# Kernel tuning notes

Hardware: AMD Instinct MI355X
Metric: run time of the kernel (lower is better)

Reference implementation:

```python
import jax, jax.numpy as jnp
import numpy as np

B, C = 4096, 1024  # batch_size, label_size (== embedding_dim of dense outputs)


def setup_inputs() -> dict:
    key = jax.random.key(0)
    k1, k2, k3 = jax.random.split(key, 3)
    return {
        "outs": jax.random.normal(k1, (B, C), dtype=jnp.float32),
        "class_centers": jax.random.normal(k2, (C, C), dtype=jnp.float32),
        "batch_label": jax.random.randint(k3, (B,), 0, C, dtype=jnp.int32),
    }


def reference(outs, class_centers, batch_label):
    b, c = outs.shape
    # ---- standard cross-entropy (F.cross_entropy, mean reduction) ----
    logp = jax.nn.log_softmax(outs, axis=-1)
    ce = -jnp.mean(jnp.take_along_axis(logp, batch_label[:, None].astype(jnp.int32), axis=1))

    # ---- InfoNCE with Wasserstein hard-negative mining ----
    # memory bank stores detached embeddings -> centers carry no gradient
    centers = jax.lax.stop_gradient(class_centers)
    pos = centers[batch_label]  # [B, C] positive per anchor

    # calculate_2_wasserstein_dist on 1-D vectors reduces EXACTLY to
    # ||x - y||^2 - 2*d*sqrt(1e-15)  (covariance terms vanish for a single column)
    const = jnp.float32(-2.0 * c * np.sqrt(1e-15))
    x = jax.lax.stop_gradient(outs)  # similarity used only for index selection
    sq = jnp.sum(x * x, axis=-1)  # [B]
    sim = sq[:, None] + sq[None, :] - 2.0 * (x @ x.T) + const  # [B, B]

    # negatives: different label (self automatically excluded: same label)
    mask = batch_label[:, None] != batch_label[None, :]  # [B, B]
    neg_inf = jnp.float32(-1e30)
    # hard negative: largest wasserstein distance among negatives (topk k=1)
    hard_idx = jnp.argmax(jnp.where(mask, sim, neg_inf), axis=1)  # [B]
    # random negative: uniform over negatives via Gumbel-max (torch randperm analogue)
    g = jax.random.gumbel(jax.random.key(42), (b, b), dtype=jnp.float32)
    rand_idx = jnp.argmax(jnp.where(mask, g, neg_inf), axis=1)  # [B]

    pos_sim = jnp.sum(outs * pos, axis=-1)                # [B]
    n_rand = jnp.sum(outs * outs[rand_idx], axis=-1)      # [B]
    n_hard = jnp.sum(outs * outs[hard_idx], axis=-1)      # [B]
    logits = jnp.stack([pos_sim, n_rand, n_hard], axis=1)  # [B, 1+num_negatives]
    info_nce = -jnp.mean(jax.nn.log_softmax(logits, axis=1)[:, 0])

    return ce + 0.1 * info_nce
```

## Files before the change

kernel.cpp:

```cpp
#include <hip/hip_runtime.h>
#include <hip/hip_bf16.h>
#include <stdint.h>

#define Bsz 4096
#define Csz 1024

typedef __attribute__((ext_vector_type(8))) short short8;
typedef __attribute__((ext_vector_type(4))) float f32x4;

__device__ __forceinline__ unsigned fenc(float v) {
  unsigned u = __float_as_uint(v);
  return (u & 0x80000000u) ? ~u : (u | 0x80000000u);
}

__device__ __forceinline__ void load_lds16(const void* g, void* l) {
  __builtin_amdgcn_global_load_lds(
      (const __attribute__((address_space(1))) void*)g,
      (__attribute__((address_space(3))) void*)l, 16, 0, 0);
}

__device__ __forceinline__ uint32_t rotl32(uint32_t x, int r) {
  return (x << r) | (x >> (32 - r));
}

__global__ __launch_bounds__(256) void k_rowstats(
    const float* __restrict__ outs, const int* __restrict__ label,
    unsigned short* __restrict__ xb, float* __restrict__ sq,
    float* __restrict__ ce) {
  const int row = blockIdx.x;
  const int tid = threadIdx.x;
  const int lane = tid & 63, wid = tid >> 6;
  const float4 v = reinterpret_cast<const float4*>(outs + (size_t)row * Csz)[tid];

  ushort4 u4;
  {
    __hip_bfloat16 h;
    h = __float2bfloat16(v.x); u4.x = *reinterpret_cast<const unsigned short*>(&h);
    h = __float2bfloat16(v.y); u4.y = *reinterpret_cast<const unsigned short*>(&h);
    h = __float2bfloat16(v.z); u4.z = *reinterpret_cast<const unsigned short*>(&h);
    h = __float2bfloat16(v.w); u4.w = *reinterpret_cast<const unsigned short*>(&h);
  }
  reinterpret_cast<ushort4*>(xb + (size_t)row * Csz)[tid] = u4;

  __shared__ float wred[3][4];
  float mx = fmaxf(fmaxf(v.x, v.y), fmaxf(v.z, v.w));
#pragma unroll
  for (int off = 32; off; off >>= 1) mx = fmaxf(mx, __shfl_xor(mx, off, 64));
  if (lane == 0) wred[0][wid] = mx;
  __syncthreads();
  mx = fmaxf(fmaxf(wred[0][0], wred[0][1]), fmaxf(wred[0][2], wred[0][3]));

  float se = expf(v.x - mx) + expf(v.y - mx) + expf(v.z - mx) + expf(v.w - mx);
  float s2 = v.x * v.x + v.y * v.y + v.z * v.z + v.w * v.w;
#pragma unroll
  for (int off = 32; off; off >>= 1) {
    se += __shfl_xor(se, off, 64);
    s2 += __shfl_xor(s2, off, 64);
  }
  if (lane == 0) { wred[1][wid] = se; wred[2][wid] = s2; }
  __syncthreads();
  if (tid == 0) {
    const float set = wred[1][0] + wred[1][1] + wred[1][2] + wred[1][3];
    const float sqt = wred[2][0] + wred[2][1] + wred[2][2] + wred[2][3];
    sq[row] = sqt;
    ce[row] = -(outs[(size_t)row * Csz + label[row]] - mx - logf(set));
  }
}

__global__ __launch_bounds__(256) void k_hard(
    const unsigned short* __restrict__ xb, const float* __restrict__ sq,
    const int* __restrict__ label, unsigned long long* __restrict__ hard) {
  __shared__ unsigned short As[128 * 64];
  __shared__ unsigned short Bs[128 * 64];

  int rem = blockIdx.x, bi = 0;
  while (rem >= 32 - bi) { rem -= 32 - bi; ++bi; }
  const int bj = bi + rem;

  const int tid = threadIdx.x;
  const int wid = tid >> 6, lane = tid & 63;
  const int wr = wid >> 1, wc = wid & 1;
  const int fr = lane & 15;
  const int fq = lane >> 4;
  const int sx = lane & 7;

  f32x4 acc[4][4];
#pragma unroll
  for (int m = 0; m < 4; ++m)
#pragma unroll
    for (int n = 0; n < 4; ++n) acc[m][n] = (f32x4){0.f, 0.f, 0.f, 0.f};

  const unsigned short* Ag = xb + (size_t)(bi * 128) * Csz;
  const unsigned short* Bg = xb + (size_t)(bj * 128) * Csz;
  const int lrow = lane >> 3;
  const int lch = ((lane & 7) ^ lrow) * 8;

  for (int kt = 0; kt < Csz; kt += 64) {
#pragma unroll
    for (int c = 0; c < 4; ++c) {
      const int r = wid * 32 + c * 8;
      load_lds16(Ag + (size_t)(r + lrow) * Csz + kt + lch, &As[r * 64]);
      load_lds16(Bg + (size_t)(r + lrow) * Csz + kt + lch, &Bs[r * 64]);
    }
    __syncthreads();
#pragma unroll
    for (int ks = 0; ks < 2; ++ks) {
      const int choff = ((ks * 4 + fq) ^ sx) * 8;
      short8 a[4], b[4];
#pragma unroll
      for (int m = 0; m < 4; ++m)
        a[m] = *reinterpret_cast<const short8*>(
            &As[(wr * 64 + m * 16 + fr) * 64 + choff]);
#pragma unroll
      for (int n = 0; n < 4; ++n)
        b[n] = *reinterpret_cast<const short8*>(
            &Bs[(wc * 64 + n * 16 + fr) * 64 + choff]);
#pragma unroll
      for (int m = 0; m < 4; ++m)
#pragma unroll
        for (int n = 0; n < 4; ++n)
          acc[m][n] = __builtin_amdgcn_mfma_f32_16x16x32_bf16(a[m], b[n], acc[m][n], 0, 0, 0);
    }
    __syncthreads();
  }

  const float cst = -2.0f * 1024.0f * 3.1622776601683794e-8f;

#pragma unroll
  for (int m = 0; m < 4; ++m) {
#pragma unroll
    for (int r = 0; r < 4; ++r) {
      const int i = bi * 128 + wr * 64 + m * 16 + fq * 4 + r;
      const int li = label[i];
      const float sqi = sq[i];
      float bestv = -3.0e38f;
      int bestj = 0x7FFFFFFF;
#pragma unroll
      for (int n = 0; n < 4; ++n) {
        const int j = bj * 128 + wc * 64 + n * 16 + fr;
        const float val = sqi + sq[j] - 2.0f * acc[m][n][r] + cst;
        if (label[j] != li && val > bestv) { bestv = val; bestj = j; }
      }
      unsigned long long pack =
          (bestj == 0x7FFFFFFF)
              ? 0ull
              : (((unsigned long long)fenc(bestv)) << 32) | (unsigned)(~bestj);
#pragma unroll
      for (int off = 1; off < 16; off <<= 1) {
        unsigned long long o = __shfl_xor(pack, off, 64);
        if (o > pack) pack = o;
      }
      if (fr == 0 && pack) atomicMax(&hard[i], pack);
    }
  }

  if (bi != bj) {
#pragma unroll
    for (int n = 0; n < 4; ++n) {
      const int j = bj * 128 + wc * 64 + n * 16 + fr;
      const int lj = label[j];
      const float sqj = sq[j];
      unsigned long long pack = 0ull;
#pragma unroll
      for (int m = 0; m < 4; ++m) {
#pragma unroll
        for (int r = 0; r < 4; ++r) {
          const int i = bi * 128 + wr * 64 + m * 16 + fq * 4 + r;
          if (label[i] != lj) {
            const float val = sq[i] + sqj - 2.0f * acc[m][n][r] + cst;
            const unsigned long long p =
                (((unsigned long long)fenc(val)) << 32) | (unsigned)(~i);
            if (p > pack) pack = p;
          }
        }
      }
      unsigned long long o;
      o = __shfl_xor(pack, 16, 64); if (o > pack) pack = o;
      o = __shfl_xor(pack, 32, 64); if (o > pack) pack = o;
      if (fq == 0 && pack) atomicMax(&hard[j], pack);
    }
  }
}

__global__ __launch_bounds__(256) void k_rand(
    const int* __restrict__ label, int* __restrict__ ridx) {
  const int i = blockIdx.x;
  const int tid = threadIdx.x;
  const int lane = tid & 63, wid = tid >> 6;
  const int li0 = label[i], li1 = label[i + 2048];
  const uint32_t k1c = 42u, k2c = 0x1BD11BDAu ^ 42u;
  unsigned long long b0 = 0ull, b1 = 0ull;
  for (int j = tid; j < Bsz; j += 256) {
    uint32_t x0 = (uint32_t)(i * Bsz + j);
    uint32_t x1 = x0 + 8388608u;
    x1 += k1c;
#define RND(rt) { x0 += x1; x1 = rotl32(x1, rt); x1 ^= x0; }
    RND(13) RND(15) RND(26) RND(6)
    x0 += k1c; x1 += k2c + 1u;
    RND(17) RND(29) RND(16) RND(24)
    x0 += k2c; x1 += 2u;
    RND(13) RND(15) RND(26) RND(6)
    x1 += k1c + 3u;
    RND(17) RND(29) RND(16) RND(24)
    x0 += k1c; x1 += k2c + 4u;
    RND(13) RND(15) RND(26) RND(6)
    x0 += k2c; x1 += 5u;
#undef RND
    const int lj = label[j];
    if (lj != li0) {
      unsigned long long p = (((unsigned long long)(x0 >> 9)) << 32) | (uint32_t)(~j);
      if (p > b0) b0 = p;
    }
    if (lj != li1) {
      unsigned long long p = (((unsigned long long)(x1 >> 9)) << 32) | (uint32_t)(~j);
      if (p > b1) b1 = p;
    }
  }
#pragma unroll
  for (int off = 32; off; off >>= 1) {
    unsigned long long o0 = __shfl_xor(b0, off, 64); if (o0 > b0) b0 = o0;
    unsigned long long o1 = __shfl_xor(b1, off, 64); if (o1 > b1) b1 = o1;
  }
  __shared__ unsigned long long r0[4], r1[4];
  if (lane == 0) { r0[wid] = b0; r1[wid] = b1; }
  __syncthreads();
  if (tid == 0) {
#pragma unroll
    for (int w = 1; w < 4; ++w) {
      if (r0[w] > b0) b0 = r0[w];
      if (r1[w] > b1) b1 = r1[w];
    }
    ridx[i] = (int)(~(uint32_t)b0);
    ridx[i + 2048] = (int)(~(uint32_t)b1);
  }
}

__global__ __launch_bounds__(256) void k_nce(
    const float* __restrict__ outs, const float* __restrict__ centers,
    const int* __restrict__ label, const unsigned long long* __restrict__ hard,
    const int* __restrict__ ridx, float* __restrict__ nce) {
  const int i = blockIdx.x;
  const int tid = threadIdx.x;
  const int lane = tid & 63, wid = tid >> 6;
  const int li = label[i];
  const int jh = (int)(~(uint32_t)hard[i]);
  const int jr = ridx[i];
  const float4 a  = reinterpret_cast<const float4*>(outs + (size_t)i * Csz)[tid];
  const float4 c  = reinterpret_cast<const float4*>(centers + (size_t)li * Csz)[tid];
  const float4 rr = reinterpret_cast<const float4*>(outs + (size_t)jr * Csz)[tid];
  const float4 hh = reinterpret_cast<const float4*>(outs + (size_t)jh * Csz)[tid];
  float dp = a.x * c.x + a.y * c.y + a.z * c.z + a.w * c.w;
  float dr = a.x * rr.x + a.y * rr.y + a.z * rr.z + a.w * rr.w;
  float dh = a.x * hh.x + a.y * hh.y + a.z * hh.z + a.w * hh.w;
#pragma unroll
  for (int off = 32; off; off >>= 1) {
    dp += __shfl_xor(dp, off, 64);
    dr += __shfl_xor(dr, off, 64);
    dh += __shfl_xor(dh, off, 64);
  }
  __shared__ float w0[4], w1[4], w2[4];
  if (lane == 0) { w0[wid] = dp; w1[wid] = dr; w2[wid] = dh; }
  __syncthreads();
  if (tid == 0) {
    const float l0 = w0[0] + w0[1] + w0[2] + w0[3];
    const float l1 = w1[0] + w1[1] + w1[2] + w1[3];
    const float l2 = w2[0] + w2[1] + w2[2] + w2[3];
    const float m = fmaxf(l0, fmaxf(l1, l2));
    const float lse = logf(expf(l0 - m) + expf(l1 - m) + expf(l2 - m));
    nce[i] = -(l0 - m - lse);
  }
}

__global__ __launch_bounds__(1024) void k_final(
    const float* __restrict__ ce, const float* __restrict__ nce,
    float* __restrict__ out) {
  __shared__ double s[1024];
  const int tid = threadIdx.x;
  double v = 0.0;
#pragma unroll
  for (int q = 0; q < 4; ++q) {
    v += (double)ce[tid + q * 1024];
    v += 0.1 * (double)nce[tid + q * 1024];
  }
  s[tid] = v;
  __syncthreads();
  for (int off = 512; off; off >>= 1) {
    if (tid < off) s[tid] += s[tid + off];
    __syncthreads();
  }
  if (tid == 0) out[0] = (float)(s[0] / 4096.0);
}

extern "C" void kernel_launch(void* const* d_in, const int* in_sizes, int n_in,
                              void* d_out, int out_size, void* d_ws, size_t ws_size,
                              hipStream_t stream) {
  const float* outs = (const float*)d_in[0];
  const float* centers = (const float*)d_in[1];
  const int* label = (const int*)d_in[2];
  float* out = (float*)d_out;

  char* ws = (char*)d_ws;
  unsigned short* xb = (unsigned short*)ws;
  unsigned long long* hard = (unsigned long long*)(ws + (8u << 20));
  float* sq = (float*)(ws + (8u << 20) + 32768);
  float* ce = sq + Bsz;
  float* nce = ce + Bsz;
  int* ridx = (int*)(nce + Bsz);

  hipMemsetAsync(hard, 0, Bsz * sizeof(unsigned long long), stream);
  k_rowstats<<<Bsz, 256, 0, stream>>>(outs, label, xb, sq, ce);
  k_hard<<<528, 256, 0, stream>>>(xb, sq, label, hard);
  k_rand<<<Bsz / 2, 256, 0, stream>>>(label, ridx);
  k_nce<<<Bsz, 256, 0, stream>>>(outs, centers, label, hard, ridx, nce);
  k_final<<<1, 1024, 0, stream>>>(ce, nce, out);
}
```

Baseline: 171.9 us.

## Fuse memset and random-negative kernel into rowstats; per-wave direct-load Gram tiles

Folds the hard-buffer zeroing and the Gumbel random-index computation into the row-stats kernel, which removes a memset and a separate launch. The Gram kernel is rewritten so each wave owns a 64x64 upper-triangular tile. Each wave loads bf16 operands straight from global memory into registers with double buffering, with no LDS or block barriers, and a swizzled block order aims to improve L2 locality. The cost is no operand sharing through LDS, so global/L2 traffic per MFMA is higher and far more atomics go out from the smaller tiles.

```diff
diff --git a/kernel.cpp b/kernel.cpp
--- a/kernel.cpp
+++ b/kernel.cpp
@@ -13,12 +13,6 @@
   return (u & 0x80000000u) ? ~u : (u | 0x80000000u);
 }
 
-__device__ __forceinline__ void load_lds16(const void* g, void* l) {
-  __builtin_amdgcn_global_load_lds(
-      (const __attribute__((address_space(1))) void*)g,
-      (__attribute__((address_space(3))) void*)l, 16, 0, 0);
-}
-
 __device__ __forceinline__ uint32_t rotl32(uint32_t x, int r) {
   return (x << r) | (x >> (32 - r));
 }
@@ -26,7 +20,8 @@
 __global__ __launch_bounds__(256) void k_rowstats(
     const float* __restrict__ outs, const int* __restrict__ label,
     unsigned short* __restrict__ xb, float* __restrict__ sq,
-    float* __restrict__ ce) {
+    float* __restrict__ ce, unsigned long long* __restrict__ hard,
+    int* __restrict__ ridx) {
   const int row = blockIdx.x;
   const int tid = threadIdx.x;
   const int lane = tid & 63, wid = tid >> 6;
@@ -64,129 +59,12 @@
     const float sqt = wred[2][0] + wred[2][1] + wred[2][2] + wred[2][3];
     sq[row] = sqt;
     ce[row] = -(outs[(size_t)row * Csz + label[row]] - mx - logf(set));
-  }
-}
-
-__global__ __launch_bounds__(256) void k_hard(
-    const unsigned short* __restrict__ xb, const float* __restrict__ sq,
-    const int* __restrict__ label, unsigned long long* __restrict__ hard) {
-  __shared__ unsigned short As[128 * 64];
-  __shared__ unsigned short Bs[128 * 64];
-
-  int rem = blockIdx.x, bi = 0;
-  while (rem >= 32 - bi) { rem -= 32 - bi; ++bi; }
-  const int bj = bi + rem;
-
-  const int tid = threadIdx.x;
-  const int wid = tid >> 6, lane = tid & 63;
-  const int wr = wid >> 1, wc = wid & 1;
-  const int fr = lane & 15;
-  const int fq = lane >> 4;
-  const int sx = lane & 7;
-
-  f32x4 acc[4][4];
-#pragma unroll
-  for (int m = 0; m < 4; ++m)
-#pragma unroll
-    for (int n = 0; n < 4; ++n) acc[m][n] = (f32x4){0.f, 0.f, 0.f, 0.f};
-
-  const unsigned short* Ag = xb + (size_t)(bi * 128) * Csz;
-  const unsigned short* Bg = xb + (size_t)(bj * 128) * Csz;
-  const int lrow = lane >> 3;
-  const int lch = ((lane & 7) ^ lrow) * 8;
-
-  for (int kt = 0; kt < Csz; kt += 64) {
-#pragma unroll
-    for (int c = 0; c < 4; ++c) {
-      const int r = wid * 32 + c * 8;
-      load_lds16(Ag + (size_t)(r + lrow) * Csz + kt + lch, &As[r * 64]);
-      load_lds16(Bg + (size_t)(r + lrow) * Csz + kt + lch, &Bs[r * 64]);
-    }
-    __syncthreads();
-#pragma unroll
-    for (int ks = 0; ks < 2; ++ks) {
-      const int choff = ((ks * 4 + fq) ^ sx) * 8;
-      short8 a[4], b[4];
-#pragma unroll
-      for (int m = 0; m < 4; ++m)
-        a[m] = *reinterpret_cast<const short8*>(
-            &As[(wr * 64 + m * 16 + fr) * 64 + choff]);
-#pragma unroll
-      for (int n = 0; n < 4; ++n)
-        b[n] = *reinterpret_cast<const short8*>(
-            &Bs[(wc * 64 + n * 16 + fr) * 64 + choff]);
-#pragma unroll
-      for (int m = 0; m < 4; ++m)
-#pragma unroll
-        for (int n = 0; n < 4; ++n)
-          acc[m][n] = __builtin_amdgcn_mfma_f32_16x16x32_bf16(a[m], b[n], acc[m][n], 0, 0, 0);
-    }
-    __syncthreads();
-  }
-
-  const float cst = -2.0f * 1024.0f * 3.1622776601683794e-8f;
-
-#pragma unroll
-  for (int m = 0; m < 4; ++m) {
-#pragma unroll
-    for (int r = 0; r < 4; ++r) {
-      const int i = bi * 128 + wr * 64 + m * 16 + fq * 4 + r;
-      const int li = label[i];
-      const float sqi = sq[i];
-      float bestv = -3.0e38f;
-      int bestj = 0x7FFFFFFF;
-#pragma unroll
-      for (int n = 0; n < 4; ++n) {
-        const int j = bj * 128 + wc * 64 + n * 16 + fr;
-        const float val = sqi + sq[j] - 2.0f * acc[m][n][r] + cst;
-        if (label[j] != li && val > bestv) { bestv = val; bestj = j; }
-      }
-      unsigned long long pack =
-          (bestj == 0x7FFFFFFF)
-              ? 0ull
-              : (((unsigned long long)fenc(bestv)) << 32) | (unsigned)(~bestj);
-#pragma unroll
-      for (int off = 1; off < 16; off <<= 1) {
-        unsigned long long o = __shfl_xor(pack, off, 64);
-        if (o > pack) pack = o;
-      }
-      if (fr == 0 && pack) atomicMax(&hard[i], pack);
-    }
-  }
-
-  if (bi != bj) {
-#pragma unroll
-    for (int n = 0; n < 4; ++n) {
-      const int j = bj * 128 + wc * 64 + n * 16 + fr;
-      const int lj = label[j];
-      const float sqj = sq[j];
-      unsigned long long pack = 0ull;
-#pragma unroll
-      for (int m = 0; m < 4; ++m) {
-#pragma unroll
-        for (int r = 0; r < 4; ++r) {
-          const int i = bi * 128 + wr * 64 + m * 16 + fq * 4 + r;
-          if (label[i] != lj) {
-            const float val = sq[i] + sqj - 2.0f * acc[m][n][r] + cst;
-            const unsigned long long p =
-                (((unsigned long long)fenc(val)) << 32) | (unsigned)(~i);
-            if (p > pack) pack = p;
-          }
-        }
-      }
-      unsigned long long o;
-      o = __shfl_xor(pack, 16, 64); if (o > pack) pack = o;
-      o = __shfl_xor(pack, 32, 64); if (o > pack) pack = o;
-      if (fq == 0 && pack) atomicMax(&hard[j], pack);
-    }
-  }
-}
-
-__global__ __launch_bounds__(256) void k_rand(
-    const int* __restrict__ label, int* __restrict__ ridx) {
-  const int i = blockIdx.x;
-  const int tid = threadIdx.x;
-  const int lane = tid & 63, wid = tid >> 6;
+    hard[row] = 0ull;
+  }
+
+  if (row >= 2048) return;
+
+  const int i = row;
   const int li0 = label[i], li1 = label[i + 2048];
   const uint32_t k1c = 42u, k2c = 0x1BD11BDAu ^ 42u;
   unsigned long long b0 = 0ull, b1 = 0ull;
@@ -235,6 +113,114 @@
   }
 }
 
+__global__ __launch_bounds__(256) void k_hard(
+    const unsigned short* __restrict__ xb, const float* __restrict__ sq,
+    const int* __restrict__ label, unsigned long long* __restrict__ hard) {
+  const int bid = (int)blockIdx.x;
+  const int swz = (bid & 7) * 65 + (bid >> 3);
+  const int gw = swz * 4 + (int)(threadIdx.x >> 6);
+  int rem = gw, bi = 0;
+  while (rem >= 64 - bi) { rem -= 64 - bi; ++bi; }
+  const int bj = bi + rem;
+
+  const int lane = (int)(threadIdx.x & 63);
+  const int fr = lane & 15;
+  const int fq = lane >> 4;
+
+  const unsigned short* Arow = xb + (size_t)(bi * 64 + fr) * Csz;
+  const unsigned short* Brow = xb + (size_t)(bj * 64 + fr) * Csz;
+
+  f32x4 acc[4][4];
+#pragma unroll
+  for (int m = 0; m < 4; ++m)
+#pragma unroll
+    for (int n = 0; n < 4; ++n) acc[m][n] = (f32x4){0.f, 0.f, 0.f, 0.f};
+
+  short8 aC[4], bC[4], aN[4], bN[4];
+
+#define LOADH(A8, B8, hh) {                                              \
+    const int ko = (hh) * 32 + fq * 8;                                   \
+    _Pragma("unroll")                                                    \
+    for (int m = 0; m < 4; ++m)                                          \
+      A8[m] = *reinterpret_cast<const short8*>(Arow + m * 16 * Csz + ko);\
+    _Pragma("unroll")                                                    \
+    for (int n = 0; n < 4; ++n)                                          \
+      B8[n] = *reinterpret_cast<const short8*>(Brow + n * 16 * Csz + ko);\
+  }
+#define MFMAH(A8, B8)                                                    \
+  _Pragma("unroll")                                                      \
+  for (int m = 0; m < 4; ++m)                                            \
+    _Pragma("unroll")                                                    \
+    for (int n = 0; n < 4; ++n)                                          \
+      acc[m][n] = __builtin_amdgcn_mfma_f32_16x16x32_bf16(A8[m], B8[n], acc[m][n], 0, 0, 0);
+
+  LOADH(aC, bC, 0);
+#pragma unroll 1
+  for (int h = 0; h < 32; h += 2) {
+    LOADH(aN, bN, h + 1);
+    MFMAH(aC, bC);
+    if (h < 30) LOADH(aC, bC, h + 2);
+    MFMAH(aN, bN);
+  }
+#undef LOADH
+#undef MFMAH
+
+  const float cst = -2.0f * 1024.0f * 3.1622776601683794e-8f;
+
+#pragma unroll
+  for (int m = 0; m < 4; ++m) {
+#pragma unroll
+    for (int r = 0; r < 4; ++r) {
+      const int i = bi * 64 + m * 16 + fq * 4 + r;
+      const int li = label[i];
+      const float sqi = sq[i];
+      float bestv = -3.0e38f;
+      int bestj = 0x7FFFFFFF;
+#pragma unroll
+      for (int n = 0; n < 4; ++n) {
+        const int j = bj * 64 + n * 16 + fr;
+        const float val = sqi + sq[j] - 2.0f * acc[m][n][r] + cst;
+        if (label[j] != li && val > bestv) { bestv = val; bestj = j; }
+      }
+      unsigned long long pack =
+          (bestj == 0x7FFFFFFF)
+              ? 0ull
+              : (((unsigned long long)fenc(bestv)) << 32) | (unsigned)(~bestj);
+#pragma unroll
+      for (int off = 1; off < 16; off <<= 1) {
+        unsigned long long o = __shfl_xor(pack, off, 64);
+        if (o > pack) pack = o;
+      }
+      if (fr == 0 && pack) atomicMax(&hard[i], pack);
+    }
+  }
+
+#pragma unroll
+  for (int n = 0; n < 4; ++n) {
+    const int j = bj * 64 + n * 16 + fr;
+    const int lj = label[j];
+    const float sqj = sq[j];
+    unsigned long long pack = 0ull;
+#pragma unroll
+    for (int m = 0; m < 4; ++m) {
+#pragma unroll
+      for (int r = 0; r < 4; ++r) {
+        const int i = bi * 64 + m * 16 + fq * 4 + r;
+        if (label[i] != lj) {
+          const float val = sq[i] + sqj - 2.0f * acc[m][n][r] + cst;
+          const unsigned long long p =
+              (((unsigned long long)fenc(val)) << 32) | (unsigned)(~i);
+          if (p > pack) pack = p;
+        }
+      }
+    }
+    unsigned long long o;
+    o = __shfl_xor(pack, 16, 64); if (o > pack) pack = o;
+    o = __shfl_xor(pack, 32, 64); if (o > pack) pack = o;
+    if (fq == 0 && pack) atomicMax(&hard[j], pack);
+  }
+}
+
 __global__ __launch_bounds__(256) void k_nce(
     const float* __restrict__ outs, const float* __restrict__ centers,
     const int* __restrict__ label, const unsigned long long* __restrict__ hard,
@@ -307,10 +293,8 @@
   float* nce = ce + Bsz;
   int* ridx = (int*)(nce + Bsz);
 
-  hipMemsetAsync(hard, 0, Bsz * sizeof(unsigned long long), stream);
-  k_rowstats<<<Bsz, 256, 0, stream>>>(outs, label, xb, sq, ce);
-  k_hard<<<528, 256, 0, stream>>>(xb, sq, label, hard);
-  k_rand<<<Bsz / 2, 256, 0, stream>>>(label, ridx);
+  k_rowstats<<<Bsz, 256, 0, stream>>>(outs, label, xb, sq, ce, hard, ridx);
+  k_hard<<<520, 256, 0, stream>>>(xb, sq, label, hard);
   k_nce<<<Bsz, 256, 0, stream>>>(outs, centers, label, hard, ridx, nce);
   k_final<<<1, 1024, 0, stream>>>(ce, nce, out);
 }
```

Result: slower. 212.2 us (+23.5%).
